# Optimization experiments

Hardware: AMD Instinct MI355X
Metric: run time of the kernel (lower is better)

## Reference

```python
import jax, jax.numpy as jnp
import numpy as np

B, N, DIM = 2, 2048, 2048
HEADS, DIM_HEAD = 16, 64
INNER = HEADS * DIM_HEAD  # 1024, != DIM -> to_out projection active
SCALE = DIM_HEAD ** -0.5


def setup_inputs() -> dict:
    key = jax.random.key(0)
    ks = jax.random.split(key, 10)
    s_in = 1.0 / np.sqrt(DIM)
    s_out = 1.0 / np.sqrt(INNER)
    return {
        "h_t": jax.random.normal(ks[0], (B, N, DIM), jnp.float32),
        "h_a": jax.random.normal(ks[1], (B, N, DIM), jnp.float32),
        "h_v": jax.random.normal(ks[2], (B, N, DIM), jnp.float32),
        "W_q": jax.random.normal(ks[3], (DIM, INNER), jnp.float32) * s_in,
        "W_k_ta": jax.random.normal(ks[4], (DIM, INNER), jnp.float32) * s_in,
        "W_k_tv": jax.random.normal(ks[5], (DIM, INNER), jnp.float32) * s_in,
        "W_v_ta": jax.random.normal(ks[6], (DIM, INNER), jnp.float32) * s_in,
        "W_v_tv": jax.random.normal(ks[7], (DIM, INNER), jnp.float32) * s_in,
        "W_out": jax.random.normal(ks[8], (INNER, DIM), jnp.float32) * s_out,
        "b_out": jnp.zeros((DIM,), jnp.float32),
    }


def _split_heads(x):
    # [b, n, h*d] -> [b, h, n, d]
    b, n, _ = x.shape
    return x.reshape(b, n, HEADS, DIM_HEAD).transpose(0, 2, 1, 3)


def _cross_attn(q, k, v):
    # q,k,v: [b, h, n, d]
    dots = jnp.einsum('bhid,bhjd->bhij', q, k) * SCALE
    attn = jax.nn.softmax(dots, axis=-1)
    out = jnp.einsum('bhij,bhjd->bhid', attn, v)
    b, h, n, d = out.shape
    return out.transpose(0, 2, 1, 3).reshape(b, n, h * d)  # [b, n, h*d]


def reference(h_t, h_a, h_v, W_q, W_k_ta, W_k_tv, W_v_ta, W_v_tv, W_out, b_out):
    q = _split_heads(h_t @ W_q)
    k_ta = _split_heads(h_a @ W_k_ta)
    v_ta = _split_heads(h_a @ W_v_ta)
    k_tv = _split_heads(h_v @ W_k_tv)
    v_tv = _split_heads(h_v @ W_v_tv)
    out_ta = _cross_attn(q, k_ta, v_ta)
    out_tv = _cross_attn(q, k_tv, v_tv)
    # project_out=True since inner_dim != dim; dropout=0 (eval)
    return h_t + (out_ta + out_tv) @ W_out + b_out
```

## Files before the change

kernel.cpp:

```cpp
#include <hip/hip_runtime.h>
#include <hip/hip_bf16.h>

typedef __attribute__((ext_vector_type(8))) short s16x8;
typedef __attribute__((ext_vector_type(4))) float f32x4;
typedef unsigned short u16;
typedef unsigned int u32;
typedef unsigned long long u64;

__device__ __forceinline__ u16 f2bf(float x) {
  __hip_bfloat16 h = __float2bfloat16(x);
  return *reinterpret_cast<u16*>(&h);
}
__device__ __forceinline__ u32 pk2(float lo, float hi) {
  return ((u32)f2bf(hi) << 16) | (u32)f2bf(lo);
}

__device__ __forceinline__ void glds16(const void* g, void* lds) {
  __builtin_amdgcn_global_load_lds(
      (const __attribute__((address_space(1))) u32*)(u64)g,
      (__attribute__((address_space(3))) u32*)(u32)(u64)lds, 16, 0, 0);
}

__global__ __launch_bounds__(256) void k_cast(const float* __restrict__ in,
                                              u16* __restrict__ out) {
  const int i = (blockIdx.x * 256 + threadIdx.x) * 8;
  float4 a = *(const float4*)(in + i);
  float4 b = *(const float4*)(in + i + 4);
  union { s16x8 v; u16 e[8]; } r;
  r.e[0] = f2bf(a.x); r.e[1] = f2bf(a.y); r.e[2] = f2bf(a.z); r.e[3] = f2bf(a.w);
  r.e[4] = f2bf(b.x); r.e[5] = f2bf(b.y); r.e[6] = f2bf(b.z); r.e[7] = f2bf(b.w);
  *(s16x8*)(out + i) = r.v;
}

__global__ __launch_bounds__(256) void k_tcast(const float* __restrict__ in,
                                               u16* __restrict__ out,
                                               int R, int C, int ldo) {
  __shared__ u16 t[64][72];
  const int tid = threadIdx.x;
  const int c0 = blockIdx.x * 64, r0 = blockIdx.y * 64;
#pragma unroll
  for (int it = 0; it < 4; ++it) {
    int c = it * 256 + tid;
    int row = c >> 4, sub = c & 15;
    float4 v = *(const float4*)(in + (u64)(r0 + row) * C + c0 + sub * 4);
    t[sub * 4 + 0][row] = f2bf(v.x);
    t[sub * 4 + 1][row] = f2bf(v.y);
    t[sub * 4 + 2][row] = f2bf(v.z);
    t[sub * 4 + 3][row] = f2bf(v.w);
  }
  __syncthreads();
#pragma unroll
  for (int it = 0; it < 2; ++it) {
    int c = it * 256 + tid;
    int orow = c >> 3, osub = c & 7;
    *(s16x8*)(out + (u64)(c0 + orow) * ldo + r0 + osub * 8) =
        *(const s16x8*)&t[orow][osub * 8];
  }
}

__global__ __launch_bounds__(256) void k_vtrans(const u16* __restrict__ kv,
                                                u16* __restrict__ vt) {
  __shared__ u16 t[64][72];
  const int bh = blockIdx.x, tb = blockIdx.y;
  const int b = bh >> 4, h = bh & 15;
  const int tid = threadIdx.x;
  const u16* src = kv + (u64)(b * 2048 + tb * 64) * 2048 + 1024 + h * 64;
#pragma unroll
  for (int it = 0; it < 2; ++it) {
    int c = it * 256 + tid;
    int trow = c >> 3, dsub = c & 7;
    union { s16x8 v; u16 e[8]; } u;
    u.v = *(const s16x8*)(src + (u64)trow * 2048 + dsub * 8);
#pragma unroll
    for (int j = 0; j < 8; ++j) t[dsub * 8 + j][trow] = u.e[j];
  }
  __syncthreads();
  u16* dst = vt + (u64)bh * 64 * 2048 + tb * 64;
#pragma unroll
  for (int it = 0; it < 2; ++it) {
    int c = it * 256 + tid;
    int drow = c >> 3, tsub = c & 7;
    *(s16x8*)(dst + (u64)drow * 2048 + tsub * 8) = *(const s16x8*)&t[drow][tsub * 8];
  }
}

template <int TM, int TN, int MODE>
__global__ __launch_bounds__(256) void k_gemm(const u16* __restrict__ A,
                                              const u16* __restrict__ Bt,
                                              void* __restrict__ Cout,
                                              const float* __restrict__ resid,
                                              const float* __restrict__ bias,
                                              int M, int N, int K, float scale) {
  constexpr int MR = TM / 32, NR = TN / 32;
  __shared__ u16 smem[(TM + TN) * 64];
  const int tid = threadIdx.x;
  const int lane = tid & 63, w = tid >> 6;
  const int g = lane >> 4, lr = lane & 15;
  const int wm = (w >> 1) * (TM / 2), wn = (w & 1) * (TN / 2);
  const int m0 = blockIdx.y * TM, n0 = blockIdx.x * TN;

  f32x4 acc[MR][NR] = {};
  int roff[2];
  roff[0] = (g * 16) ^ ((lr & 7) << 4);
  roff[1] = (64 + g * 16) ^ ((lr & 7) << 4);

  const int nkt = K >> 6;
  for (int kt = 0; kt < nkt; ++kt) {
    const int k0 = kt << 6;
#pragma unroll
    for (int it = 0; it < (TM + TN) / 32; ++it) {
      int c = it * 256 + tid;
      int p = c * 16;
      const u16* gsrc;
      if (c < TM * 8) {
        int lby = p ^ (((p >> 7) & 7) << 4);
        gsrc = A + (u64)(m0 + (lby >> 7)) * K + k0 + ((lby >> 4) & 7) * 8;
      } else {
        int pb = p - TM * 128;
        int lby = pb ^ (((pb >> 7) & 7) << 4);
        gsrc = Bt + (u64)(n0 + (lby >> 7)) * K + k0 + ((lby >> 4) & 7) * 8;
      }
      glds16(gsrc, (char*)smem + p);
    }
    __syncthreads();
#pragma unroll
    for (int ks = 0; ks < 2; ++ks) {
      s16x8 a[MR], b[NR];
#pragma unroll
      for (int m = 0; m < MR; ++m)
        a[m] = *(const s16x8*)((const char*)smem + (wm + m * 16 + lr) * 128 + roff[ks]);
#pragma unroll
      for (int n = 0; n < NR; ++n)
        b[n] = *(const s16x8*)((const char*)smem + TM * 128 + (wn + n * 16 + lr) * 128 + roff[ks]);
#pragma unroll
      for (int m = 0; m < MR; ++m)
#pragma unroll
        for (int n = 0; n < NR; ++n)
          acc[m][n] = __builtin_amdgcn_mfma_f32_16x16x32_bf16(a[m], b[n], acc[m][n], 0, 0, 0);
    }
    __syncthreads();
  }

#pragma unroll
  for (int m = 0; m < MR; ++m)
#pragma unroll
    for (int n = 0; n < NR; ++n) {
      const int col = n0 + wn + n * 16 + lr;
#pragma unroll
      for (int r = 0; r < 4; ++r) {
        const int row = m0 + wm + m * 16 + g * 4 + r;
        if constexpr (MODE == 0) {
          ((u16*)Cout)[(u64)row * N + col] = f2bf(acc[m][n][r]);
        } else if constexpr (MODE == 2) {
          ((u16*)Cout)[(u64)row * N + col] = f2bf(acc[m][n][r] * scale);
        } else {
          ((float*)Cout)[(u64)row * N + col] =
              acc[m][n][r] + resid[(u64)row * N + col] + bias[col];
        }
      }
    }
}

__global__ __launch_bounds__(512, 6) void k_attn(const u16* __restrict__ Q,
                                                 const u16* __restrict__ Kta,
                                                 const u16* __restrict__ Ktv,
                                                 const u16* __restrict__ VTta,
                                                 const u16* __restrict__ VTtv,
                                                 u16* __restrict__ AO) {
  const int bx = blockIdx.x;
  const int br = bx & 1, bh = bx >> 1;
  const int b = bh >> 4, h = bh & 15;
  const int qb = blockIdx.y;
  const int tid = threadIdx.x, lane = tid & 63, w = tid >> 6;
  const int g = lane >> 4, q = lane & 15;
  const int qrow = b * 2048 + qb * 128 + w * 16;
  const int bh64 = bh * 64;
  const u16* Kp  = br ? Ktv  : Kta;
  const u16* VTp = br ? VTtv : VTta;

  __shared__ __align__(16) char sbuf[2][16384];
  __shared__ u32 pbuf[8][16][32];

  s16x8 qf[2];
#pragma unroll
  for (int ks = 0; ks < 2; ++ks)
    qf[ks] = *(const s16x8*)(Q + (u64)(qrow + q) * 1024 + h * 64 + ks * 32 + g * 8);

  const int sp = tid * 16;
  const int slby = sp ^ (((sp >> 7) & 7) << 4);
  const int srow = slby >> 7, scol = (slby & 127) >> 1;

  {
    glds16(Kp + (u64)(b * 2048 + 0 + srow) * 2048 + h * 64 + scol, sbuf[0] + sp);
    glds16(VTp + (u64)(bh64 + srow) * 2048 + 0 + scol, sbuf[0] + 8192 + sp);
  }
  __syncthreads();

  float lsum = 0.f;
  f32x4 acco[4] = {};
  const int xsw = (q & 7) << 4;
  const int psw = (q & 7) << 2;

  for (int t = 0; t < 32; ++t) {
    const int cur = t & 1;
    if (t + 1 < 32) {
      const int kv1 = (t + 1) * 64;
      glds16(Kp + (u64)(b * 2048 + kv1 + srow) * 2048 + h * 64 + scol,
             sbuf[cur ^ 1] + sp);
      glds16(VTp + (u64)(bh64 + srow) * 2048 + kv1 + scol,
             sbuf[cur ^ 1] + 8192 + sp);
    }

    f32x4 s[4];
    __builtin_amdgcn_s_setprio(1);
#pragma unroll
    for (int n = 0; n < 4; ++n) {
      const char* base = sbuf[cur] + (16 * n + q) * 128;
      s16x8 kf0 = *(const s16x8*)(base + ((16 * g) ^ xsw));
      s16x8 kf1 = *(const s16x8*)(base + ((64 + 16 * g) ^ xsw));
      f32x4 z = {};
      z = __builtin_amdgcn_mfma_f32_16x16x32_bf16(kf0, qf[0], z, 0, 0, 0);
      s[n] = __builtin_amdgcn_mfma_f32_16x16x32_bf16(kf1, qf[1], z, 0, 0, 0);
    }
    __builtin_amdgcn_s_setprio(0);

#pragma unroll
    for (int n = 0; n < 4; ++n) {
#pragma unroll
      for (int r = 0; r < 4; ++r) s[n][r] = __builtin_amdgcn_exp2f(s[n][r]);
      lsum += (s[n][0] + s[n][1]) + (s[n][2] + s[n][3]);
      pbuf[w][q][(8 * n + 2 * g) ^ psw]     = pk2(s[n][0], s[n][1]);
      pbuf[w][q][(8 * n + 2 * g + 1) ^ psw] = pk2(s[n][2], s[n][3]);
    }
    s16x8 pb[2];
#pragma unroll
    for (int ks = 0; ks < 2; ++ks)
      pb[ks] = *(const s16x8*)&pbuf[w][q][(16 * ks + 4 * g) ^ psw];

    __builtin_amdgcn_s_setprio(1);
#pragma unroll
    for (int n = 0; n < 4; ++n) {
      const char* base = sbuf[cur] + 8192 + (16 * n + q) * 128;
      s16x8 v0 = *(const s16x8*)(base + ((16 * g) ^ xsw));
      s16x8 v1 = *(const s16x8*)(base + ((64 + 16 * g) ^ xsw));
      acco[n] = __builtin_amdgcn_mfma_f32_16x16x32_bf16(v0, pb[0], acco[n], 0, 0, 0);
      acco[n] = __builtin_amdgcn_mfma_f32_16x16x32_bf16(v1, pb[1], acco[n], 0, 0, 0);
    }
    __builtin_amdgcn_s_setprio(0);
    __syncthreads();
  }

  lsum += __shfl_xor(lsum, 16);
  lsum += __shfl_xor(lsum, 32);
  const float inv = 1.0f / lsum;

#pragma unroll
  for (int n = 0; n < 4; ++n) {
    pbuf[w][q][(8 * n + 2 * g) ^ psw]     = pk2(acco[n][0] * inv, acco[n][1] * inv);
    pbuf[w][q][(8 * n + 2 * g + 1) ^ psw] = pk2(acco[n][2] * inv, acco[n][3] * inv);
  }
#pragma unroll
  for (int c = 0; c < 2; ++c) {
    const int row = (lane >> 3) + 8 * c;
    const int wc = (lane & 7) * 4;
    s16x8 vv = *(const s16x8*)&pbuf[w][row][wc ^ ((row & 7) << 2)];
    *(s16x8*)(AO + (u64)(b * 2048 + qb * 128 + w * 16 + row) * 2048 +
              br * 1024 + h * 64 + (lane & 7) * 8) = vv;
  }
}

extern "C" void kernel_launch(void* const* d_in, const int* in_sizes, int n_in,
                              void* d_out, int out_size, void* d_ws, size_t ws_size,
                              hipStream_t stream) {
  (void)in_sizes; (void)n_in; (void)out_size; (void)ws_size;
  const float* h_t    = (const float*)d_in[0];
  const float* h_a    = (const float*)d_in[1];
  const float* h_v    = (const float*)d_in[2];
  const float* W_q    = (const float*)d_in[3];
  const float* W_k_ta = (const float*)d_in[4];
  const float* W_k_tv = (const float*)d_in[5];
  const float* W_v_ta = (const float*)d_in[6];
  const float* W_v_tv = (const float*)d_in[7];
  const float* W_out  = (const float*)d_in[8];
  const float* b_out  = (const float*)d_in[9];
  float* out = (float*)d_out;

  const float CEXP = 0.125f * 1.44269504088896f;

  u16* ws    = (u16*)d_ws;
  u16* hT    = ws;
  u16* hA    = hT + 8388608;
  u16* hV    = hA + 8388608;
  u16* WqT   = hV + 8388608;
  u16* WkvTa = WqT + 2097152;
  u16* WkvTv = WkvTa + 4194304;
  u16* WoT2  = WkvTv + 4194304;
  u16* Qb    = WoT2 + 4194304;
  u16* KVta  = Qb + 4194304;
  u16* KVtv  = KVta + 8388608;
  u16* VTta  = KVtv + 8388608;
  u16* VTtv  = VTta + 4194304;
  u16* AO    = hT;

  k_cast<<<4096, 256, 0, stream>>>(h_t, hT);
  k_cast<<<4096, 256, 0, stream>>>(h_a, hA);
  k_cast<<<4096, 256, 0, stream>>>(h_v, hV);

  dim3 g1(16, 32);
  k_tcast<<<g1, 256, 0, stream>>>(W_q,    WqT,                 2048, 1024, 2048);
  k_tcast<<<g1, 256, 0, stream>>>(W_k_ta, WkvTa,               2048, 1024, 2048);
  k_tcast<<<g1, 256, 0, stream>>>(W_v_ta, WkvTa + 1024 * 2048, 2048, 1024, 2048);
  k_tcast<<<g1, 256, 0, stream>>>(W_k_tv, WkvTv,               2048, 1024, 2048);
  k_tcast<<<g1, 256, 0, stream>>>(W_v_tv, WkvTv + 1024 * 2048, 2048, 1024, 2048);
  dim3 g2(32, 16);
  k_tcast<<<g2, 256, 0, stream>>>(W_out, WoT2,        1024, 2048, 2048);
  k_tcast<<<g2, 256, 0, stream>>>(W_out, WoT2 + 1024, 1024, 2048, 2048);

  k_gemm<64, 128, 2><<<dim3(8, 64), 256, 0, stream>>>(hT, WqT, Qb, nullptr, nullptr, 4096, 1024, 2048, CEXP);
  k_gemm<128, 128, 0><<<dim3(16, 32), 256, 0, stream>>>(hA, WkvTa, KVta, nullptr, nullptr, 4096, 2048, 2048, 1.0f);
  k_gemm<128, 128, 0><<<dim3(16, 32), 256, 0, stream>>>(hV, WkvTv, KVtv, nullptr, nullptr, 4096, 2048, 2048, 1.0f);

  k_vtrans<<<dim3(32, 32), 256, 0, stream>>>(KVta, VTta);
  k_vtrans<<<dim3(32, 32), 256, 0, stream>>>(KVtv, VTtv);

  k_attn<<<dim3(64, 16), 512, 0, stream>>>(Qb, KVta, KVtv, VTta, VTtv, AO);

  k_gemm<128, 128, 1><<<dim3(16, 32), 256, 0, stream>>>(AO, WoT2, out, h_t, b_out, 4096, 2048, 1024 * 2, 1.0f);
}
```

Before: 343.8 us.

## Process two query tiles per attention block to reuse K/V LDS tiles

After: 383.9 us. 11.7% more time.

```diff
diff --git a/kernel.cpp b/kernel.cpp
--- a/kernel.cpp
+++ b/kernel.cpp
@@ -161,7 +161,7 @@
     }
 }
 
-__global__ __launch_bounds__(512, 6) void k_attn(const u16* __restrict__ Q,
+__global__ __launch_bounds__(512, 4) void k_attn(const u16* __restrict__ Q,
                                                  const u16* __restrict__ Kta,
                                                  const u16* __restrict__ Ktv,
                                                  const u16* __restrict__ VTta,
@@ -173,7 +173,7 @@
   const int qb = blockIdx.y;
   const int tid = threadIdx.x, lane = tid & 63, w = tid >> 6;
   const int g = lane >> 4, q = lane & 15;
-  const int qrow = b * 2048 + qb * 128 + w * 16;
+  const int qrow0 = b * 2048 + qb * 256 + w * 16;
   const int bh64 = bh * 64;
   const u16* Kp  = br ? Ktv  : Kta;
   const u16* VTp = br ? VTtv : VTta;
@@ -181,10 +181,13 @@
   __shared__ __align__(16) char sbuf[2][16384];
   __shared__ u32 pbuf[8][16][32];
 
-  s16x8 qf[2];
-#pragma unroll
-  for (int ks = 0; ks < 2; ++ks)
-    qf[ks] = *(const s16x8*)(Q + (u64)(qrow + q) * 1024 + h * 64 + ks * 32 + g * 8);
+  s16x8 qf[2][2];
+#pragma unroll
+  for (int u = 0; u < 2; ++u)
+#pragma unroll
+    for (int ks = 0; ks < 2; ++ks)
+      qf[u][ks] = *(const s16x8*)(Q + (u64)(qrow0 + u * 128 + q) * 1024 +
+                                  h * 64 + ks * 32 + g * 8);
 
   const int sp = tid * 16;
   const int slby = sp ^ (((sp >> 7) & 7) << 4);
@@ -196,8 +199,8 @@
   }
   __syncthreads();
 
-  float lsum = 0.f;
-  f32x4 acco[4] = {};
+  float lsum[2] = {0.f, 0.f};
+  f32x4 acco[2][4] = {};
   const int xsw = (q & 7) << 4;
   const int psw = (q & 7) << 2;
 
@@ -211,61 +214,67 @@
              sbuf[cur ^ 1] + 8192 + sp);
     }
 
-    f32x4 s[4];
-    __builtin_amdgcn_s_setprio(1);
+#pragma unroll
+    for (int u = 0; u < 2; ++u) {
+      f32x4 s[4];
+      __builtin_amdgcn_s_setprio(1);
+#pragma unroll
+      for (int n = 0; n < 4; ++n) {
+        const char* base = sbuf[cur] + (16 * n + q) * 128;
+        s16x8 kf0 = *(const s16x8*)(base + ((16 * g) ^ xsw));
+        s16x8 kf1 = *(const s16x8*)(base + ((64 + 16 * g) ^ xsw));
+        f32x4 z = {};
+        z = __builtin_amdgcn_mfma_f32_16x16x32_bf16(kf0, qf[u][0], z, 0, 0, 0);
+        s[n] = __builtin_amdgcn_mfma_f32_16x16x32_bf16(kf1, qf[u][1], z, 0, 0, 0);
+      }
+      __builtin_amdgcn_s_setprio(0);
+
+#pragma unroll
+      for (int n = 0; n < 4; ++n) {
+#pragma unroll
+        for (int r = 0; r < 4; ++r) s[n][r] = __builtin_amdgcn_exp2f(s[n][r]);
+        lsum[u] += (s[n][0] + s[n][1]) + (s[n][2] + s[n][3]);
+        pbuf[w][q][(8 * n + 2 * g) ^ psw]     = pk2(s[n][0], s[n][1]);
+        pbuf[w][q][(8 * n + 2 * g + 1) ^ psw] = pk2(s[n][2], s[n][3]);
+      }
+      s16x8 pb[2];
+#pragma unroll
+      for (int ks = 0; ks < 2; ++ks)
+        pb[ks] = *(const s16x8*)&pbuf[w][q][(16 * ks + 4 * g) ^ psw];
+
+      __builtin_amdgcn_s_setprio(1);
+#pragma unroll
+      for (int n = 0; n < 4; ++n) {
+        const char* base = sbuf[cur] + 8192 + (16 * n + q) * 128;
+        s16x8 v0 = *(const s16x8*)(base + ((16 * g) ^ xsw));
+        s16x8 v1 = *(const s16x8*)(base + ((64 + 16 * g) ^ xsw));
+        acco[u][n] = __builtin_amdgcn_mfma_f32_16x16x32_bf16(v0, pb[0], acco[u][n], 0, 0, 0);
+        acco[u][n] = __builtin_amdgcn_mfma_f32_16x16x32_bf16(v1, pb[1], acco[u][n], 0, 0, 0);
+      }
+      __builtin_amdgcn_s_setprio(0);
+    }
+    __syncthreads();
+  }
+
+#pragma unroll
+  for (int u = 0; u < 2; ++u) {
+    float ls = lsum[u];
+    ls += __shfl_xor(ls, 16);
+    ls += __shfl_xor(ls, 32);
+    const float inv = 1.0f / ls;
 #pragma unroll
     for (int n = 0; n < 4; ++n) {
-      const char* base = sbuf[cur] + (16 * n + q) * 128;
-      s16x8 kf0 = *(const s16x8*)(base + ((16 * g) ^ xsw));
-      s16x8 kf1 = *(const s16x8*)(base + ((64 + 16 * g) ^ xsw));
-      f32x4 z = {};
-      z = __builtin_amdgcn_mfma_f32_16x16x32_bf16(kf0, qf[0], z, 0, 0, 0);
-      s[n] = __builtin_amdgcn_mfma_f32_16x16x32_bf16(kf1, qf[1], z, 0, 0, 0);
-    }
-    __builtin_amdgcn_s_setprio(0);
-
-#pragma unroll
-    for (int n = 0; n < 4; ++n) {
-#pragma unroll
-      for (int r = 0; r < 4; ++r) s[n][r] = __builtin_amdgcn_exp2f(s[n][r]);
-      lsum += (s[n][0] + s[n][1]) + (s[n][2] + s[n][3]);
-      pbuf[w][q][(8 * n + 2 * g) ^ psw]     = pk2(s[n][0], s[n][1]);
-      pbuf[w][q][(8 * n + 2 * g + 1) ^ psw] = pk2(s[n][2], s[n][3]);
-    }
-    s16x8 pb[2];
-#pragma unroll
-    for (int ks = 0; ks < 2; ++ks)
-      pb[ks] = *(const s16x8*)&pbuf[w][q][(16 * ks + 4 * g) ^ psw];
-
-    __builtin_amdgcn_s_setprio(1);
-#pragma unroll
-    for (int n = 0; n < 4; ++n) {
-      const char* base = sbuf[cur] + 8192 + (16 * n + q) * 128;
-      s16x8 v0 = *(const s16x8*)(base + ((16 * g) ^ xsw));
-      s16x8 v1 = *(const s16x8*)(base + ((64 + 16 * g) ^ xsw));
-      acco[n] = __builtin_amdgcn_mfma_f32_16x16x32_bf16(v0, pb[0], acco[n], 0, 0, 0);
-      acco[n] = __builtin_amdgcn_mfma_f32_16x16x32_bf16(v1, pb[1], acco[n], 0, 0, 0);
-    }
-    __builtin_amdgcn_s_setprio(0);
-    __syncthreads();
-  }
-
-  lsum += __shfl_xor(lsum, 16);
-  lsum += __shfl_xor(lsum, 32);
-  const float inv = 1.0f / lsum;
-
-#pragma unroll
-  for (int n = 0; n < 4; ++n) {
-    pbuf[w][q][(8 * n + 2 * g) ^ psw]     = pk2(acco[n][0] * inv, acco[n][1] * inv);
-    pbuf[w][q][(8 * n + 2 * g + 1) ^ psw] = pk2(acco[n][2] * inv, acco[n][3] * inv);
-  }
-#pragma unroll
-  for (int c = 0; c < 2; ++c) {
-    const int row = (lane >> 3) + 8 * c;
-    const int wc = (lane & 7) * 4;
-    s16x8 vv = *(const s16x8*)&pbuf[w][row][wc ^ ((row & 7) << 2)];
-    *(s16x8*)(AO + (u64)(b * 2048 + qb * 128 + w * 16 + row) * 2048 +
-              br * 1024 + h * 64 + (lane & 7) * 8) = vv;
+      pbuf[w][q][(8 * n + 2 * g) ^ psw]     = pk2(acco[u][n][0] * inv, acco[u][n][1] * inv);
+      pbuf[w][q][(8 * n + 2 * g + 1) ^ psw] = pk2(acco[u][n][2] * inv, acco[u][n][3] * inv);
+    }
+#pragma unroll
+    for (int c = 0; c < 2; ++c) {
+      const int row = (lane >> 3) + 8 * c;
+      const int wc = (lane & 7) * 4;
+      s16x8 vv = *(const s16x8*)&pbuf[w][row][wc ^ ((row & 7) << 2)];
+      *(s16x8*)(AO + (u64)(qrow0 + u * 128 + row) * 2048 +
+                br * 1024 + h * 64 + (lane & 7) * 8) = vv;
+    }
   }
 }
 
@@ -323,7 +332,7 @@
   k_vtrans<<<dim3(32, 32), 256, 0, stream>>>(KVta, VTta);
   k_vtrans<<<dim3(32, 32), 256, 0, stream>>>(KVtv, VTtv);
 
-  k_attn<<<dim3(64, 16), 512, 0, stream>>>(Qb, KVta, KVtv, VTta, VTtv, AO);
+  k_attn<<<dim3(64, 8), 512, 0, stream>>>(Qb, KVta, KVtv, VTta, VTtv, AO);
 
   k_gemm<128, 128, 1><<<dim3(16, 32), 256, 0, stream>>>(AO, WoT2, out, h_t, b_out, 4096, 2048, 1024 * 2, 1.0f);
 }
```

## Fuse prep kernels into one launch and pre-add attention outputs before projection

Applied to the files above, without the earlier changes.

Measured after the change: 302.5 us. 1.14x faster.

```diff
diff --git a/kernel.cpp b/kernel.cpp
--- a/kernel.cpp
+++ b/kernel.cpp
@@ -11,6 +11,9 @@
   __hip_bfloat16 h = __float2bfloat16(x);
   return *reinterpret_cast<u16*>(&h);
 }
+__device__ __forceinline__ float bf2f(u16 x) {
+  union { u32 u; float f; } c; c.u = ((u32)x) << 16; return c.f;
+}
 __device__ __forceinline__ u32 pk2(float lo, float hi) {
   return ((u32)f2bf(hi) << 16) | (u32)f2bf(lo);
 }
@@ -21,23 +24,12 @@
       (__attribute__((address_space(3))) u32*)(u32)(u64)lds, 16, 0, 0);
 }
 
-__global__ __launch_bounds__(256) void k_cast(const float* __restrict__ in,
-                                              u16* __restrict__ out) {
-  const int i = (blockIdx.x * 256 + threadIdx.x) * 8;
-  float4 a = *(const float4*)(in + i);
-  float4 b = *(const float4*)(in + i + 4);
-  union { s16x8 v; u16 e[8]; } r;
-  r.e[0] = f2bf(a.x); r.e[1] = f2bf(a.y); r.e[2] = f2bf(a.z); r.e[3] = f2bf(a.w);
-  r.e[4] = f2bf(b.x); r.e[5] = f2bf(b.y); r.e[6] = f2bf(b.z); r.e[7] = f2bf(b.w);
-  *(s16x8*)(out + i) = r.v;
-}
-
-__global__ __launch_bounds__(256) void k_tcast(const float* __restrict__ in,
-                                               u16* __restrict__ out,
-                                               int R, int C, int ldo) {
-  __shared__ u16 t[64][72];
-  const int tid = threadIdx.x;
-  const int c0 = blockIdx.x * 64, r0 = blockIdx.y * 64;
+__device__ __forceinline__ void tcast_tile(const float* __restrict__ in,
+                                           u16* __restrict__ out,
+                                           int R, int C, int ldo,
+                                           int bx, int by, int tid,
+                                           u16 (*t)[72]) {
+  const int c0 = bx * 64, r0 = by * 64;
 #pragma unroll
   for (int it = 0; it < 4; ++it) {
     int c = it * 256 + tid;
@@ -58,10 +50,54 @@
   }
 }
 
-__global__ __launch_bounds__(256) void k_vtrans(const u16* __restrict__ kv,
-                                                u16* __restrict__ vt) {
+__global__ __launch_bounds__(256) void k_prep(
+    const float* __restrict__ h_t, const float* __restrict__ h_a,
+    const float* __restrict__ h_v, const float* __restrict__ W_q,
+    const float* __restrict__ W_k_ta, const float* __restrict__ W_v_ta,
+    const float* __restrict__ W_k_tv, const float* __restrict__ W_v_tv,
+    const float* __restrict__ W_out, u16* __restrict__ hT,
+    u16* __restrict__ hA, u16* __restrict__ hV, u16* __restrict__ WqT,
+    u16* __restrict__ WkvTa, u16* __restrict__ WkvTv, u16* __restrict__ WoT) {
   __shared__ u16 t[64][72];
-  const int bh = blockIdx.x, tb = blockIdx.y;
+  const int bid = blockIdx.x, tid = threadIdx.x;
+  if (bid < 12288) {
+    const float* in = bid < 4096 ? h_t : bid < 8192 ? h_a : h_v;
+    u16* out = bid < 4096 ? hT : bid < 8192 ? hA : hV;
+    const int i = (bid & 4095) * 2048 + tid * 8;
+    float4 a = *(const float4*)(in + i);
+    float4 b = *(const float4*)(in + i + 4);
+    union { s16x8 v; u16 e[8]; } r;
+    r.e[0] = f2bf(a.x); r.e[1] = f2bf(a.y); r.e[2] = f2bf(a.z); r.e[3] = f2bf(a.w);
+    r.e[4] = f2bf(b.x); r.e[5] = f2bf(b.y); r.e[6] = f2bf(b.z); r.e[7] = f2bf(b.w);
+    *(s16x8*)(out + i) = r.v;
+  } else if (bid < 14848) {
+    const int tt = bid - 12288;
+    const int wi = tt / 512, t2 = tt % 512;
+    const float* in;
+    u16* out;
+    switch (wi) {
+      case 0: in = W_q;    out = WqT; break;
+      case 1: in = W_k_ta; out = WkvTa; break;
+      case 2: in = W_v_ta; out = WkvTa + 1024 * 2048; break;
+      case 3: in = W_k_tv; out = WkvTv; break;
+      default: in = W_v_tv; out = WkvTv + 1024 * 2048; break;
+    }
+    tcast_tile(in, out, 2048, 1024, 2048, t2 % 16, t2 / 16, tid, t);
+  } else {
+    const int t2 = bid - 14848;
+    tcast_tile(W_out, WoT, 1024, 2048, 1024, t2 % 32, t2 / 32, tid, t);
+  }
+}
+
+__global__ __launch_bounds__(256) void k_vtrans2(const u16* __restrict__ kva,
+                                                 const u16* __restrict__ kvv,
+                                                 u16* __restrict__ vta,
+                                                 u16* __restrict__ vtv) {
+  __shared__ u16 t[64][72];
+  const int bx = blockIdx.x, tb = blockIdx.y;
+  const int bh = bx & 31;
+  const u16* kv = (bx < 32) ? kva : kvv;
+  u16* vt = (bx < 32) ? vta : vtv;
   const int b = bh >> 4, h = bh & 15;
   const int tid = threadIdx.x;
   const u16* src = kv + (u64)(b * 2048 + tb * 64) * 2048 + 1024 + h * 64;
@@ -82,6 +118,18 @@
     int drow = c >> 3, tsub = c & 7;
     *(s16x8*)(dst + (u64)drow * 2048 + tsub * 8) = *(const s16x8*)&t[drow][tsub * 8];
   }
+}
+
+__global__ __launch_bounds__(256) void k_add(const u16* __restrict__ ao,
+                                             u16* __restrict__ aoc) {
+  const int i = blockIdx.x * 2048 + threadIdx.x * 8;
+  const int row = i >> 10, col = i & 1023;
+  union { s16x8 v; u16 e[8]; } A, B, O;
+  A.v = *(const s16x8*)(ao + (u64)row * 2048 + col);
+  B.v = *(const s16x8*)(ao + (u64)row * 2048 + 1024 + col);
+#pragma unroll
+  for (int j = 0; j < 8; ++j) O.e[j] = f2bf(bf2f(A.e[j]) + bf2f(B.e[j]));
+  *(s16x8*)(aoc + (u64)row * 1024 + col) = O.v;
 }
 
 template <int TM, int TN, int MODE>
@@ -294,36 +342,28 @@
   u16* WqT   = hV + 8388608;
   u16* WkvTa = WqT + 2097152;
   u16* WkvTv = WkvTa + 4194304;
-  u16* WoT2  = WkvTv + 4194304;
-  u16* Qb    = WoT2 + 4194304;
+  u16* WoT   = WkvTv + 4194304;
+  u16* Qb    = WoT + 2097152;
   u16* KVta  = Qb + 4194304;
   u16* KVtv  = KVta + 8388608;
   u16* VTta  = KVtv + 8388608;
   u16* VTtv  = VTta + 4194304;
   u16* AO    = hT;
-
-  k_cast<<<4096, 256, 0, stream>>>(h_t, hT);
-  k_cast<<<4096, 256, 0, stream>>>(h_a, hA);
-  k_cast<<<4096, 256, 0, stream>>>(h_v, hV);
-
-  dim3 g1(16, 32);
-  k_tcast<<<g1, 256, 0, stream>>>(W_q,    WqT,                 2048, 1024, 2048);
-  k_tcast<<<g1, 256, 0, stream>>>(W_k_ta, WkvTa,               2048, 1024, 2048);
-  k_tcast<<<g1, 256, 0, stream>>>(W_v_ta, WkvTa + 1024 * 2048, 2048, 1024, 2048);
-  k_tcast<<<g1, 256, 0, stream>>>(W_k_tv, WkvTv,               2048, 1024, 2048);
-  k_tcast<<<g1, 256, 0, stream>>>(W_v_tv, WkvTv + 1024 * 2048, 2048, 1024, 2048);
-  dim3 g2(32, 16);
-  k_tcast<<<g2, 256, 0, stream>>>(W_out, WoT2,        1024, 2048, 2048);
-  k_tcast<<<g2, 256, 0, stream>>>(W_out, WoT2 + 1024, 1024, 2048, 2048);
+  u16* AOc   = hA;
+
+  k_prep<<<15360, 256, 0, stream>>>(h_t, h_a, h_v, W_q, W_k_ta, W_v_ta,
+                                    W_k_tv, W_v_tv, W_out,
+                                    hT, hA, hV, WqT, WkvTa, WkvTv, WoT);
 
   k_gemm<64, 128, 2><<<dim3(8, 64), 256, 0, stream>>>(hT, WqT, Qb, nullptr, nullptr, 4096, 1024, 2048, CEXP);
   k_gemm<128, 128, 0><<<dim3(16, 32), 256, 0, stream>>>(hA, WkvTa, KVta, nullptr, nullptr, 4096, 2048, 2048, 1.0f);
   k_gemm<128, 128, 0><<<dim3(16, 32), 256, 0, stream>>>(hV, WkvTv, KVtv, nullptr, nullptr, 4096, 2048, 2048, 1.0f);
 
-  k_vtrans<<<dim3(32, 32), 256, 0, stream>>>(KVta, VTta);
-  k_vtrans<<<dim3(32, 32), 256, 0, stream>>>(KVtv, VTtv);
+  k_vtrans2<<<dim3(64, 32), 256, 0, stream>>>(KVta, KVtv, VTta, VTtv);
 
   k_attn<<<dim3(64, 16), 512, 0, stream>>>(Qb, KVta, KVtv, VTta, VTtv, AO);
 
-  k_gemm<128, 128, 1><<<dim3(16, 32), 256, 0, stream>>>(AO, WoT2, out, h_t, b_out, 4096, 2048, 1024 * 2, 1.0f);
-}
+  k_add<<<2048, 256, 0, stream>>>(AO, AOc);
+
+  k_gemm<128, 128, 1><<<dim3(16, 32), 256, 0, stream>>>(AOc, WoT, out, h_t, b_out, 4096, 2048, 1024, 1.0f);
+}
```
